# Performance work log

Measured on AMD Instinct MI355X. Metric: run time of the kernel, lower is better.

Reference implementation:

```python
import jax, jax.numpy as jnp
import numpy as np

N, D, E, R, TOPK = 8192, 4096, 8, 128, 2
LORA_ALPHA = 32.0
SCALING = LORA_ALPHA / R


def setup_inputs() -> dict:
    key = jax.random.key(0)
    kx, kr, ka, kb = jax.random.split(key, 4)
    x = jax.random.normal(kx, (N, D), jnp.float32)
    Wr = jax.random.normal(kr, (E, D), jnp.float32) * 0.02  # router Linear weight [E, D]
    br = jnp.zeros((E,), jnp.float32)                        # router bias
    A = jax.random.normal(ka, (E, R, D), jnp.float32) * 0.02  # per-expert lora_A weights
    B = jax.random.normal(kb, (E, D, R), jnp.float32) * 0.02  # per-expert lora_B weights
    return {"x": x, "Wr": Wr, "br": br, "A": A, "B": B}


def reference(x, Wr, br, A, B):
    # Router: softmax over expert logits, top-k, renormalize selected probs.
    logits = x @ Wr.T + br                       # [N, E]
    probs = jax.nn.softmax(logits, axis=-1)
    top_v, top_i = jax.lax.top_k(probs, TOPK)    # [N, K]
    w = top_v / jnp.sum(top_v, axis=-1, keepdims=True)
    # Scatter renormalized weights back to a dense [N, E] gate (0 for unselected).
    n_idx = jnp.arange(x.shape[0])[:, None]
    gate = jnp.zeros_like(probs).at[n_idx, top_i].set(w)
    # Expert LoRA: y_e = (x @ A_e^T) @ B_e^T * scaling; combine with gates.
    h = jnp.einsum('nd,erd->ner', x, A)          # [N, E, R] small rank intermediate
    out = jnp.einsum('ner,ne,eor->no', h, gate, B) * SCALING  # [N, D]
    return out
```

## Files before the change

kernel.cpp:

```cpp
#include <hip/hip_runtime.h>

#define N_TOK 8192
#define DIM   4096
#define NEXP  8
#define RANK  128
#define EK    (NEXP * RANK)
#define SCAL  0.25f

typedef unsigned short u16;
typedef __bf16 bf16x8 __attribute__((ext_vector_type(8)));
typedef float  f32x4  __attribute__((ext_vector_type(4)));

typedef const __attribute__((address_space(1))) void* as1_cvp;
typedef __attribute__((address_space(3))) void*       as3_vp;

__device__ __forceinline__ void async16(void* lds, const void* g) {
  __builtin_amdgcn_global_load_lds((as1_cvp)g, (as3_vp)lds, 16, 0, 0);
}

__device__ __forceinline__ u16 f2bf(float f) {
  unsigned int u = __builtin_bit_cast(unsigned int, f);
  u += 0x7fffu + ((u >> 16) & 1u);
  return (u16)(u >> 16);
}

__device__ __forceinline__ f32x4 mfma16(bf16x8 a, bf16x8 b, f32x4 c) {
  return __builtin_amdgcn_mfma_f32_16x16x32_bf16(a, b, c, 0, 0, 0);
}

#define PIPE_WAIT(N)                                            \
  __builtin_amdgcn_sched_barrier(0);                            \
  asm volatile("s_waitcnt vmcnt(" #N ")" ::: "memory");         \
  __builtin_amdgcn_s_barrier();                                 \
  __builtin_amdgcn_sched_barrier(0)

#define PIPE_END()                                              \
  __builtin_amdgcn_sched_barrier(0);                            \
  __builtin_amdgcn_s_barrier();                                 \
  __builtin_amdgcn_sched_barrier(0)

__global__ __launch_bounds__(256) void cvtA_kernel(const float* __restrict__ A,
                                                   u16* __restrict__ Ab) {
  size_t i = (size_t)blockIdx.x * 256 + threadIdx.x;
  float4 v = ((const float4*)A)[i];
  ushort4 o;
  o.x = f2bf(v.x); o.y = f2bf(v.y); o.z = f2bf(v.z); o.w = f2bf(v.w);
  ((ushort4*)Ab)[i] = o;
}

__global__ __launch_bounds__(256) void cvtB_kernel(const float* __restrict__ B,
                                                   u16* __restrict__ Bt) {
  size_t i = (size_t)blockIdx.x * 256 + threadIdx.x;
  int r4 = (int)(i & 31);
  int o_ = (int)((i >> 5) & 4095);
  int e  = (int)(i >> 17);
  float4 v = ((const float4*)B)[i];
  ushort4 u;
  u.x = f2bf(v.x); u.y = f2bf(v.y); u.z = f2bf(v.z); u.w = f2bf(v.w);
  ((ushort4*)Bt)[(size_t)o_ * 256 + e * 32 + r4] = u;
}

__device__ __forceinline__ void router_finalize(
    int n, const float* l_in, const float* __restrict__ br,
    float* __restrict__ gw, int* __restrict__ sel) {
  float l[NEXP];
#pragma unroll
  for (int e = 0; e < NEXP; ++e) l[e] = l_in[e] + br[e];
  int i0 = 0;
#pragma unroll
  for (int e = 1; e < NEXP; ++e) if (l[e] > l[i0]) i0 = e;
  int i1 = (i0 == 0) ? 1 : 0;
#pragma unroll
  for (int e = 0; e < NEXP; ++e) if (e != i0 && l[e] > l[i1]) i1 = e;
  float w0 = 1.f / (1.f + expf(l[i1] - l[i0]));
  gw[n * 2 + 0] = w0 * SCAL;
  gw[n * 2 + 1] = (1.f - w0) * SCAL;
  sel[n] = i0 | (i1 << 4);
}

__global__ __launch_bounds__(256) void router_kernel(
    const float* __restrict__ x, const float* __restrict__ Wr,
    const float* __restrict__ br, u16* __restrict__ xb,
    float* __restrict__ gw, int* __restrict__ sel) {
  const int tid = threadIdx.x;
  const int wv = tid >> 6, lane = tid & 63;
  const int n0 = (blockIdx.x * 4 + wv) * 2;
  const float4* x4 = (const float4*)x;
  const float4* w4 = (const float4*)Wr;

  const float4* xr0 = x4 + (size_t)n0 * 1024;
  const float4* xr1 = x4 + (size_t)(n0 + 1) * 1024;
  ushort4* xo0 = (ushort4*)(xb + (size_t)n0 * DIM);
  ushort4* xo1 = (ushort4*)(xb + (size_t)(n0 + 1) * DIM);

  float s0[NEXP] = {}, s1[NEXP] = {};
#pragma unroll 4
  for (int it = 0; it < 16; ++it) {
    const int col = it * 64 + lane;
    float4 xv0 = xr0[col];
    float4 xv1 = xr1[col];
    ushort4 o0, o1;
    o0.x = f2bf(xv0.x); o0.y = f2bf(xv0.y); o0.z = f2bf(xv0.z); o0.w = f2bf(xv0.w);
    o1.x = f2bf(xv1.x); o1.y = f2bf(xv1.y); o1.z = f2bf(xv1.z); o1.w = f2bf(xv1.w);
    xo0[col] = o0;
    xo1[col] = o1;
#pragma unroll
    for (int e = 0; e < NEXP; ++e) {
      float4 wv4 = w4[(size_t)e * 1024 + col];
      s0[e] += xv0.x * wv4.x + xv0.y * wv4.y + xv0.z * wv4.z + xv0.w * wv4.w;
      s1[e] += xv1.x * wv4.x + xv1.y * wv4.y + xv1.z * wv4.z + xv1.w * wv4.w;
    }
  }
#pragma unroll
  for (int m = 1; m < 64; m <<= 1)
#pragma unroll
    for (int e = 0; e < NEXP; ++e) {
      s0[e] += __shfl_xor(s0[e], m, 64);
      s1[e] += __shfl_xor(s1[e], m, 64);
    }
  if (lane == 0)      router_finalize(n0,     s0, br, gw, sel);
  else if (lane == 1) router_finalize(n0 + 1, s1, br, gw, sel);
}

__global__ __launch_bounds__(512) void listbuild_kernel(
    const int* __restrict__ sel, int* __restrict__ lists,
    int* __restrict__ cnt) {
  __shared__ int blkCnt[NEXP];
  __shared__ int gBase[NEXP];
  __shared__ int waveOff[8][NEXP];
  const int tid = threadIdx.x;
  const int wv = tid >> 6, lane = tid & 63;
  const int n = blockIdx.x * 512 + tid;
  if (tid < NEXP) blkCnt[tid] = 0;
  __syncthreads();
  const int s = sel[n];
  const int i0 = s & 15, i1 = (s >> 4) & 15;
#pragma unroll
  for (int e = 0; e < NEXP; ++e) {
    unsigned long long m0 = __ballot(i0 == e);
    unsigned long long m1 = __ballot(i1 == e);
    if (lane == 0)
      waveOff[wv][e] = atomicAdd(&blkCnt[e], __popcll(m0) + __popcll(m1));
  }
  __syncthreads();
  if (tid < NEXP) gBase[tid] = atomicAdd(&cnt[tid], blkCnt[tid]);
  __syncthreads();
  const unsigned long long lt = (1ull << lane) - 1;
#pragma unroll
  for (int e = 0; e < NEXP; ++e) {
    unsigned long long m0 = __ballot(i0 == e);
    unsigned long long m1 = __ballot(i1 == e);
    int base = gBase[e] + waveOff[wv][e];
    if (i0 == e) lists[e * N_TOK + base + (int)__popcll(m0 & lt)] = n * 2;
    if (i1 == e)
      lists[e * N_TOK + base + (int)__popcll(m0) + (int)__popcll(m1 & lt)] =
          n * 2 + 1;
  }
}

__global__ __launch_bounds__(256) void gemm1_kernel(
    const u16* __restrict__ xb, const u16* __restrict__ Ab,
    const int* __restrict__ lists, const int* __restrict__ cnt,
    const float* __restrict__ gw, u16* __restrict__ G) {
  const int e = blockIdx.y;
  const int mt = blockIdx.x;
  const int c = cnt[e];
  if (mt * 64 >= c) return;

  __shared__ alignas(16) u16 ringA[4][64 * 32];
  __shared__ alignas(16) u16 ringB[4][128 * 32];
  __shared__ int   tokS[64];
  __shared__ float wS[64];

  const int tid = threadIdx.x;
  if (tid < 64) {
    int idx = mt * 64 + tid;
    int ci = idx < c ? idx : (c - 1);
    int entry = lists[e * N_TOK + ci];
    tokS[tid] = entry >> 1;
    wS[tid] = (idx < c) ? gw[entry] : 0.0f;
  }
  __syncthreads();

  const int srow = tid >> 2;
  const int scol = (tid & 3) * 8;
  const u16* gA  = xb + (size_t)tokS[srow] * DIM + scol;
  const u16* gB0 = Ab + (size_t)e * (RANK * DIM) + (size_t)srow * DIM + scol;
  const u16* gB1 = gB0 + (size_t)64 * DIM;

  const int lane = tid & 63, wvi = tid >> 6;
  const int wm = wvi >> 1, wn = wvi & 1;
  const int m16 = lane & 15, quad = lane >> 4;

  f32x4 acc[2][4] = {};

  auto STAGE = [&](int kt, int slot) {
    const int k0 = kt * 32;
    async16(&ringA[slot][tid * 8],        gA  + k0);
    async16(&ringB[slot][tid * 8],        gB0 + k0);
    async16(&ringB[slot][tid * 8 + 2048], gB1 + k0);
  };

  auto COMPUTE = [&](int slot) {
    bf16x8 af[2], bfr[4];
#pragma unroll
    for (int j = 0; j < 4; ++j)
      bfr[j] = *(const bf16x8*)&ringB[slot][(wn * 64 + j * 16 + m16) * 32 + quad * 8];
#pragma unroll
    for (int i = 0; i < 2; ++i)
      af[i] = *(const bf16x8*)&ringA[slot][(wm * 32 + i * 16 + m16) * 32 + quad * 8];
    __builtin_amdgcn_s_setprio(1);
#pragma unroll
    for (int i = 0; i < 2; ++i)
#pragma unroll
      for (int j = 0; j < 4; ++j) acc[i][j] = mfma16(af[i], bfr[j], acc[i][j]);
    __builtin_amdgcn_s_setprio(0);
  };

  STAGE(0, 0);
  STAGE(1, 1);
  STAGE(2, 2);

  for (int t = 0; t < 125; ++t) {
    PIPE_WAIT(6);
    STAGE(t + 3, (t + 3) & 3);
    COMPUTE(t & 3);
    PIPE_END();
  }
  PIPE_WAIT(6); COMPUTE(1); PIPE_END();
  PIPE_WAIT(3); COMPUTE(2); PIPE_END();
  PIPE_WAIT(0); COMPUTE(3); PIPE_END();

#pragma unroll
  for (int i = 0; i < 2; ++i)
#pragma unroll
    for (int rr = 0; rr < 4; ++rr) {
      int row = wm * 32 + i * 16 + quad * 4 + rr;
      if (mt * 64 + row < c) {
        int tk = tokS[row];
        float wgt = wS[row];
        u16* gp = G + (size_t)tk * EK + e * RANK + wn * 64 + m16;
#pragma unroll
        for (int j = 0; j < 4; ++j) gp[j * 16] = f2bf(acc[i][j][rr] * wgt);
      }
    }
}

__global__ __launch_bounds__(512, 2) void gemm2_kernel(
    const u16* __restrict__ G, const u16* __restrict__ Bt,
    float* __restrict__ out) {
  __shared__ alignas(16) u16 ring[4][2][256 * 32];

  const int lin = blockIdx.y * 16 + blockIdx.x;
  const int swz = (lin & 7) * 64 + (lin >> 3);
  const int by = swz >> 4;
  const int bx = swz & 15;

  const int tid = threadIdx.x;
  const int sr = tid >> 2;
  const int sc = (tid & 3) * 8;
  const u16* gA = G  + (size_t)(by * 256 + sr) * EK + sc;
  const u16* gB = Bt + (size_t)(bx * 256 + sr) * EK + sc;

  const int lane = tid & 63, wvi = tid >> 6;
  const int wm = wvi >> 2, wn = wvi & 3;
  const int m16 = lane & 15, quad = lane >> 4;

  f32x4 acc[8][4] = {};

  auto STAGE = [&](int kt, int slot) {
    u16* lA = &ring[slot][0][tid * 8];
    u16* lB = &ring[slot][1][tid * 8];
    const u16* sA = gA + kt * 32;
    const u16* sB = gB + kt * 32;
    async16(lA,        sA);
    async16(lA + 4096, sA + (size_t)128 * EK);
    async16(lB,        sB);
    async16(lB + 4096, sB + (size_t)128 * EK);
  };

  auto COMPUTE = [&](int slot) {
    const u16* As_ = &ring[slot][0][0];
    const u16* Bs_ = &ring[slot][1][0];
    bf16x8 bfr[4];
#pragma unroll
    for (int j = 0; j < 4; ++j)
      bfr[j] = *(const bf16x8*)&Bs_[(wn * 64 + j * 16 + m16) * 32 + quad * 8];
    __builtin_amdgcn_s_setprio(1);
#pragma unroll
    for (int i = 0; i < 8; ++i) {
      bf16x8 af = *(const bf16x8*)&As_[(wm * 128 + i * 16 + m16) * 32 + quad * 8];
#pragma unroll
      for (int j = 0; j < 4; ++j) acc[i][j] = mfma16(af, bfr[j], acc[i][j]);
    }
    __builtin_amdgcn_s_setprio(0);
  };

  STAGE(0, 0);
  STAGE(1, 1);
  STAGE(2, 2);

  for (int t = 0; t < 29; ++t) {
    PIPE_WAIT(8);
    STAGE(t + 3, (t + 3) & 3);
    COMPUTE(t & 3);
    PIPE_END();
  }
  PIPE_WAIT(8); COMPUTE(1); PIPE_END();
  PIPE_WAIT(4); COMPUTE(2); PIPE_END();
  PIPE_WAIT(0); COMPUTE(3); PIPE_END();

#pragma unroll
  for (int i = 0; i < 8; ++i)
#pragma unroll
    for (int rr = 0; rr < 4; ++rr) {
      int row = by * 256 + wm * 128 + i * 16 + quad * 4 + rr;
      float* op = out + (size_t)row * DIM + bx * 256 + wn * 64 + m16;
#pragma unroll
      for (int j = 0; j < 4; ++j) op[j * 16] = acc[i][j][rr];
    }
}

extern "C" void kernel_launch(void* const* d_in, const int* in_sizes, int n_in,
                              void* d_out, int out_size, void* d_ws, size_t ws_size,
                              hipStream_t stream) {
  const float* x  = (const float*)d_in[0];
  const float* Wr = (const float*)d_in[1];
  const float* br = (const float*)d_in[2];
  const float* A  = (const float*)d_in[3];
  const float* B  = (const float*)d_in[4];
  float* out = (float*)d_out;

  char* w = (char*)d_ws;
  u16* xb = (u16*)w;      w += (size_t)N_TOK * DIM * 2;
  u16* G  = (u16*)w;      w += (size_t)N_TOK * EK * 2;
  u16* Ab = (u16*)w;      w += (size_t)NEXP * RANK * DIM * 2;
  u16* Bt = (u16*)w;      w += (size_t)DIM * EK * 2;
  float* gw = (float*)w;  w += (size_t)N_TOK * 2 * 4;
  int* lists = (int*)w;   w += (size_t)NEXP * N_TOK * 4;
  int* sel = (int*)w;     w += (size_t)N_TOK * 4;
  int* cnt = (int*)w;     w += 256;

  hipMemsetAsync(cnt, 0, NEXP * sizeof(int), stream);
  hipMemsetAsync(G, 0, (size_t)N_TOK * EK * 2, stream);

  cvtA_kernel<<<dim3(4096), dim3(256), 0, stream>>>(A, Ab);
  cvtB_kernel<<<dim3(4096), dim3(256), 0, stream>>>(B, Bt);
  router_kernel<<<dim3(1024), dim3(256), 0, stream>>>(x, Wr, br, xb, gw, sel);
  listbuild_kernel<<<dim3(16), dim3(512), 0, stream>>>(sel, lists, cnt);
  gemm1_kernel<<<dim3(128, NEXP), dim3(256), 0, stream>>>(xb, Ab, lists, cnt, gw, G);
  gemm2_kernel<<<dim3(16, 32), dim3(512), 0, stream>>>(G, Bt, out);
}
```

Measured before the change: 446.7 us.

## Stage router weights in LDS with double-buffered async loads, four tokens per wave

The router kernel now has each wave process four tokens instead of two. Router weight chunks are staged into double-buffered LDS with async global-to-LDS loads, and x chunks are prefetched into registers one stage ahead so loads overlap the dot-product work. This reuses each Wr chunk across 16 tokens per block and halves the grid size. In exchange it raises register pressure and uses 32KB of LDS per block, which can cut occupancy on a kernel that is bound by memory bandwidth.

New measurement: 446.3 us. No clear change (-0.1%).

```diff
diff --git a/kernel.cpp b/kernel.cpp
--- a/kernel.cpp
+++ b/kernel.cpp
@@ -78,48 +78,107 @@
   sel[n] = i0 | (i1 << 4);
 }
 
-__global__ __launch_bounds__(256) void router_kernel(
+#define R_STAGE(kc, buf)                                                    \
+  {                                                                         \
+    const int k0_ = (kc) * 512;                                             \
+    _Pragma("unroll")                                                       \
+    for (int r_ = 0; r_ < 4; ++r_)                                          \
+      async16(&WrL[buf][r_ * 1024 + tid * 4],                               \
+              wsrc + (size_t)(2 * r_) * DIM + k0_);                         \
+  }
+
+#define R_LOADX(kc, xv)                                                     \
+  {                                                                         \
+    const int kb_ = (kc) * 128;                                             \
+    _Pragma("unroll")                                                       \
+    for (int t_ = 0; t_ < 4; ++t_)                                          \
+      _Pragma("unroll")                                                     \
+      for (int c_ = 0; c_ < 2; ++c_)                                        \
+        xv[t_][c_] = x4[(size_t)(tok0 + t_) * 1024 + kb_ + c_ * 64 + lane]; \
+  }
+
+#define R_COMPUTE(kc, buf, xv)                                              \
+  {                                                                         \
+    const float4* WL_ = (const float4*)WrL[buf];                            \
+    _Pragma("unroll")                                                       \
+    for (int c_ = 0; c_ < 2; ++c_) {                                        \
+      float4 wr_[8];                                                        \
+      _Pragma("unroll")                                                     \
+      for (int e_ = 0; e_ < 8; ++e_)                                        \
+        wr_[e_] = WL_[e_ * 128 + c_ * 64 + lane];                           \
+      _Pragma("unroll")                                                     \
+      for (int t_ = 0; t_ < 4; ++t_)                                        \
+        _Pragma("unroll")                                                   \
+        for (int e_ = 0; e_ < 8; ++e_)                                      \
+          sums[t_][e_] += xv[t_][c_].x * wr_[e_].x + xv[t_][c_].y * wr_[e_].y + \
+                          xv[t_][c_].z * wr_[e_].z + xv[t_][c_].w * wr_[e_].w;  \
+    }                                                                       \
+    const int kb_ = (kc) * 128;                                             \
+    _Pragma("unroll")                                                       \
+    for (int t_ = 0; t_ < 4; ++t_) {                                        \
+      ushort4* xo_ = (ushort4*)(xb + (size_t)(tok0 + t_) * DIM);            \
+      _Pragma("unroll")                                                     \
+      for (int c_ = 0; c_ < 2; ++c_) {                                      \
+        float4 v_ = xv[t_][c_];                                             \
+        ushort4 o_;                                                         \
+        o_.x = f2bf(v_.x); o_.y = f2bf(v_.y);                               \
+        o_.z = f2bf(v_.z); o_.w = f2bf(v_.w);                               \
+        xo_[kb_ + c_ * 64 + lane] = o_;                                     \
+      }                                                                     \
+    }                                                                       \
+  }
+
+__global__ __launch_bounds__(256, 2) void router_kernel(
     const float* __restrict__ x, const float* __restrict__ Wr,
     const float* __restrict__ br, u16* __restrict__ xb,
     float* __restrict__ gw, int* __restrict__ sel) {
+  __shared__ alignas(16) float WrL[2][4096];
+
   const int tid = threadIdx.x;
   const int wv = tid >> 6, lane = tid & 63;
-  const int n0 = (blockIdx.x * 4 + wv) * 2;
+  const int tok0 = blockIdx.x * 16 + wv * 4;
+
   const float4* x4 = (const float4*)x;
-  const float4* w4 = (const float4*)Wr;
-
-  const float4* xr0 = x4 + (size_t)n0 * 1024;
-  const float4* xr1 = x4 + (size_t)(n0 + 1) * 1024;
-  ushort4* xo0 = (ushort4*)(xb + (size_t)n0 * DIM);
-  ushort4* xo1 = (ushort4*)(xb + (size_t)(n0 + 1) * DIM);
-
-  float s0[NEXP] = {}, s1[NEXP] = {};
-#pragma unroll 4
-  for (int it = 0; it < 16; ++it) {
-    const int col = it * 64 + lane;
-    float4 xv0 = xr0[col];
-    float4 xv1 = xr1[col];
-    ushort4 o0, o1;
-    o0.x = f2bf(xv0.x); o0.y = f2bf(xv0.y); o0.z = f2bf(xv0.z); o0.w = f2bf(xv0.w);
-    o1.x = f2bf(xv1.x); o1.y = f2bf(xv1.y); o1.z = f2bf(xv1.z); o1.w = f2bf(xv1.w);
-    xo0[col] = o0;
-    xo1[col] = o1;
-#pragma unroll
-    for (int e = 0; e < NEXP; ++e) {
-      float4 wv4 = w4[(size_t)e * 1024 + col];
-      s0[e] += xv0.x * wv4.x + xv0.y * wv4.y + xv0.z * wv4.z + xv0.w * wv4.w;
-      s1[e] += xv1.x * wv4.x + xv1.y * wv4.y + xv1.z * wv4.z + xv1.w * wv4.w;
-    }
-  }
+  const float* wsrc = Wr + (size_t)(tid >> 7) * DIM + (tid & 127) * 4;
+
+  float4 xvA[4][2], xvB[4][2];
+  float sums[4][8] = {};
+
+  R_STAGE(0, 0); R_LOADX(0, xvA);
+  for (int kc = 0; kc < 3; ++kc) {
+    R_STAGE(2 * kc + 1, 1); R_LOADX(2 * kc + 1, xvB);
+    PIPE_WAIT(12);
+    R_COMPUTE(2 * kc, 0, xvA);
+    PIPE_END();
+    R_STAGE(2 * kc + 2, 0); R_LOADX(2 * kc + 2, xvA);
+    PIPE_WAIT(12);
+    R_COMPUTE(2 * kc + 1, 1, xvB);
+    PIPE_END();
+  }
+  R_STAGE(7, 1); R_LOADX(7, xvB);
+  PIPE_WAIT(12);
+  R_COMPUTE(6, 0, xvA);
+  PIPE_END();
+  PIPE_WAIT(0);
+  R_COMPUTE(7, 1, xvB);
+
 #pragma unroll
   for (int m = 1; m < 64; m <<= 1)
 #pragma unroll
-    for (int e = 0; e < NEXP; ++e) {
-      s0[e] += __shfl_xor(s0[e], m, 64);
-      s1[e] += __shfl_xor(s1[e], m, 64);
-    }
-  if (lane == 0)      router_finalize(n0,     s0, br, gw, sel);
-  else if (lane == 1) router_finalize(n0 + 1, s1, br, gw, sel);
+    for (int t = 0; t < 4; ++t)
+#pragma unroll
+      for (int e = 0; e < 8; ++e)
+        sums[t][e] += __shfl_xor(sums[t][e], m, 64);
+
+  if (lane < 4) {
+    float fl[8];
+#pragma unroll
+    for (int e = 0; e < 8; ++e)
+      fl[e] = lane == 0 ? sums[0][e]
+            : lane == 1 ? sums[1][e]
+            : lane == 2 ? sums[2][e] : sums[3][e];
+    router_finalize(tok0 + lane, fl, br, gw, sel);
+  }
 }
 
 __global__ __launch_bounds__(512) void listbuild_kernel(
@@ -346,7 +405,7 @@
 
   cvtA_kernel<<<dim3(4096), dim3(256), 0, stream>>>(A, Ab);
   cvtB_kernel<<<dim3(4096), dim3(256), 0, stream>>>(B, Bt);
-  router_kernel<<<dim3(1024), dim3(256), 0, stream>>>(x, Wr, br, xb, gw, sel);
+  router_kernel<<<dim3(512), dim3(256), 0, stream>>>(x, Wr, br, xb, gw, sel);
   listbuild_kernel<<<dim3(16), dim3(512), 0, stream>>>(sel, lists, cnt);
   gemm1_kernel<<<dim3(128, NEXP), dim3(256), 0, stream>>>(xb, Ab, lists, cnt, gw, G);
   gemm2_kernel<<<dim3(16, 32), dim3(512), 0, stream>>>(G, Bt, out);
```
